# Kernel tuning notes

Measured on AMD Instinct MI355X. Metric: run time of the kernel, lower is better.

The kernel has to match this reference:

```python
import jax, jax.numpy as jnp
import numpy as np

N_NODES = 100000
N_EDGES = 1600000
D_IN = 128
D_OUT = 128


def setup_inputs() -> dict:
    key = jax.random.key(0)
    ks = jax.random.split(key, 6)
    x = jax.random.normal(ks[0], (N_NODES, D_IN), dtype=jnp.float32)
    edge_row = jax.random.randint(ks[1], (N_EDGES,), 0, N_NODES, dtype=jnp.int32)
    edge_col = jax.random.randint(ks[2], (N_EDGES,), 0, N_NODES, dtype=jnp.int32)
    # normalized adjacency values (e.g. 1/deg), roughly uniform small positives
    edge_val = jax.random.uniform(ks[3], (N_EDGES,), dtype=jnp.float32) * (1.0 / 16.0)
    # torch Linear weight is [out,in]; we store transposed [in,out] for x @ W
    scale = float(np.sqrt(6.0 / (D_IN + D_OUT)))  # xavier_uniform
    W_local = jax.random.uniform(ks[4], (D_IN, D_OUT), dtype=jnp.float32, minval=-scale, maxval=scale)
    W_neigh = jax.random.uniform(ks[5], (D_IN, D_OUT), dtype=jnp.float32, minval=-scale, maxval=scale)
    b_local = jnp.zeros((D_OUT,), dtype=jnp.float32)
    b_neigh = jnp.zeros((D_OUT,), dtype=jnp.float32)
    return {"x": x, "edge_row": edge_row, "edge_col": edge_col, "edge_val": edge_val,
            "W_local": W_local, "b_local": b_local, "W_neigh": W_neigh, "b_neigh": b_neigh}


def reference(x, edge_row, edge_col, edge_val, W_local, b_local, W_neigh, b_neigh):
    # feat_trans_local = linear_local(x)
    local = x @ W_local + b_local  # [N, D_OUT]
    # sparse.mm(edge_norm, x): out[r] += val * x[c]  (COO SpMM via gather + segment_sum)
    msgs = edge_val[:, None] * x[edge_col]  # [E, D_IN]
    agg = jax.ops.segment_sum(msgs, edge_row, num_segments=N_NODES)  # [N, D_IN]
    neigh = agg @ W_neigh + b_neigh  # [N, D_OUT]
    out = jnp.concatenate([local, neigh], axis=1)  # [N, 2*D_OUT]
    return jax.nn.relu(out)
```

## Files before the change

kernel.cpp:

```cpp
#include <hip/hip_runtime.h>
#include <hip/hip_bf16.h>

#define D 128
#define WPAD 136
#define RPC 64
#define RPC_SHIFT 6
#define CAPC 1280
#define NCMAX 2048
#define P1_BLOCKS 256

typedef __attribute__((ext_vector_type(8))) short short8;
typedef __attribute__((ext_vector_type(4))) short sh4;
typedef __attribute__((ext_vector_type(8))) __bf16 bf16x8;
typedef __attribute__((ext_vector_type(4))) float float4_t;

__device__ __forceinline__ short f2bf(float f) {
    __hip_bfloat16 b = __float2bfloat16(f);
    return __builtin_bit_cast(short, b);
}

__device__ __forceinline__ short8 load_frag8(const float* p) {
    const float4_t* q = reinterpret_cast<const float4_t*>(p);
    float4_t u = q[0], v = q[1];
    short8 r;
    r[0] = f2bf(u[0]); r[1] = f2bf(u[1]); r[2] = f2bf(u[2]); r[3] = f2bf(u[3]);
    r[4] = f2bf(v[0]); r[5] = f2bf(v[1]); r[6] = f2bf(v[2]); r[7] = f2bf(v[3]);
    return r;
}

__device__ __forceinline__ float4_t mfma_bf16(short8 a, short8 b, float4_t c) {
    return __builtin_amdgcn_mfma_f32_16x16x32_bf16(
        __builtin_bit_cast(bf16x8, a), __builtin_bit_cast(bf16x8, b), c, 0, 0, 0);
}

__device__ __forceinline__ float bf_lo(unsigned u) { return __uint_as_float(u << 16); }
__device__ __forceinline__ float bf_hi(unsigned u) { return __uint_as_float(u & 0xFFFF0000u); }

__global__ __launch_bounds__(256) void fused_gemm_scatter(
    const float* __restrict__ x,
    const float* __restrict__ Wl, const float* __restrict__ bl,
    const float* __restrict__ Wn,
    const int* __restrict__ erow, const int* __restrict__ ecol,
    const float* __restrict__ eval,
    float* __restrict__ out, unsigned short* __restrict__ y,
    int* __restrict__ gcur, int2* __restrict__ pairs1,
    int E, int ncoarse, int N)
{
    __shared__ int smem[D * WPAD / 2];

    if (blockIdx.x < P1_BLOCKS) {
        int* hist = smem;
        int* base = smem + NCMAX;
        int tid = threadIdx.x;
        for (int i = tid; i < ncoarse; i += 256) hist[i] = 0;
        __syncthreads();

        int chunk = (E + P1_BLOCKS - 1) / P1_BLOCKS;
        int e0 = blockIdx.x * chunk;
        int e1 = e0 + chunk; e1 = e1 < E ? e1 : E;

        for (int e = e0 + tid; e < e1; e += 256)
            atomicAdd(&hist[erow[e] >> RPC_SHIFT], 1);
        __syncthreads();

        for (int i = tid; i < ncoarse; i += 256) {
            int h = hist[i];
            base[i] = h ? atomicAdd(&gcur[i], h) : 0;
            hist[i] = 0;
        }
        __syncthreads();

        for (int e = e0 + tid; e < e1; e += 256) {
            int r = erow[e];
            int c = r >> RPC_SHIFT;
            int pos = atomicAdd(&hist[c], 1) + base[c];
            if (pos < CAPC) {
                int key = ((r & (RPC - 1)) << 17) | ecol[e];
                pairs1[(size_t)c * CAPC + pos] = make_int2(key, __float_as_int(eval[e]));
            }
        }
        return;
    }

    short* lW = reinterpret_cast<short*>(smem);
    int gb = blockIdx.x - P1_BLOCKS;

    for (int i = threadIdx.x; i < D * D; i += 256) {
        int k = i >> 7, n = i & (D - 1);
        lW[n * WPAD + k] = f2bf(Wl[i]);
    }

    int wave = threadIdx.x >> 6;
    int lane = threadIdx.x & 63;
    int quad = lane >> 4;
    int l16  = lane & 15;
    int rbase = gb * 128 + wave * 32;

    short8 ax[2][4];
    for (int m = 0; m < 2; ++m) {
        int row  = rbase + m * 16 + l16;
        int rowc = row < N ? row : N - 1;
        const float* xp = x + (size_t)rowc * D + quad * 8;
        for (int t = 0; t < 4; ++t) ax[m][t] = load_frag8(xp + t * 32);
    }
    __syncthreads();

    for (int nt = 0; nt < 8; ++nt) {
        int colc = nt * 16 + l16;
        float4_t acc0 = {0.f, 0.f, 0.f, 0.f};
        float4_t acc1 = {0.f, 0.f, 0.f, 0.f};
        const short* bp = lW + colc * WPAD + quad * 8;
        for (int t = 0; t < 4; ++t) {
            short8 bf = *reinterpret_cast<const short8*>(bp + t * 32);
            acc0 = mfma_bf16(bf, ax[0][t], acc0);
            acc1 = mfma_bf16(bf, ax[1][t], acc1);
        }
        float4_t blv = *reinterpret_cast<const float4_t*>(bl + nt * 16 + quad * 4);
        int col0 = nt * 16 + quad * 4;
        for (int m = 0; m < 2; ++m) {
            int row = rbase + m * 16 + l16;
            if (row < N) {
                float4_t a = m ? acc1 : acc0;
                float4_t ov;
                #pragma unroll
                for (int i = 0; i < 4; ++i) {
                    float lv = a[i] + blv[i];
                    ov[i] = lv > 0.f ? lv : 0.f;
                }
                *reinterpret_cast<float4_t*>(out + (size_t)row * 256 + col0) = ov;
            }
        }
    }
    __syncthreads();

    for (int i = threadIdx.x; i < D * D; i += 256) {
        int k = i >> 7, n = i & (D - 1);
        lW[n * WPAD + k] = f2bf(Wn[i]);
    }
    __syncthreads();

    for (int nt = 0; nt < 8; ++nt) {
        int colc = nt * 16 + l16;
        float4_t acc0 = {0.f, 0.f, 0.f, 0.f};
        float4_t acc1 = {0.f, 0.f, 0.f, 0.f};
        const short* bp = lW + colc * WPAD + quad * 8;
        for (int t = 0; t < 4; ++t) {
            short8 bf = *reinterpret_cast<const short8*>(bp + t * 32);
            acc0 = mfma_bf16(bf, ax[0][t], acc0);
            acc1 = mfma_bf16(bf, ax[1][t], acc1);
        }
        int col0 = nt * 16 + quad * 4;
        for (int m = 0; m < 2; ++m) {
            int row = rbase + m * 16 + l16;
            if (row < N) {
                float4_t a = m ? acc1 : acc0;
                sh4 s;
                #pragma unroll
                for (int i = 0; i < 4; ++i) s[i] = f2bf(a[i]);
                *reinterpret_cast<sh4*>(y + (size_t)row * 128 + col0) = s;
            }
        }
    }
}

__global__ __launch_bounds__(256) void bucket_gather(
    const unsigned short* __restrict__ y, const int* __restrict__ gcur,
    const int2* __restrict__ pairs1, const float* __restrict__ bn,
    float* __restrict__ out, int N)
{
    __shared__ unsigned short bidx[CAPC];
    __shared__ int hist[32];
    __shared__ int off[32];
    __shared__ int cur[32];

    int tid  = threadIdx.x;
    int wave = tid >> 6;
    int lane = tid & 63;
    int b    = blockIdx.x;
    int c    = b >> 1;
    int half = b & 1;

    if (tid < 32) { hist[tid] = 0; cur[tid] = 0; }
    __syncthreads();

    int cnt = gcur[c];
    cnt = cnt < CAPC ? cnt : CAPC;
    const int2* pb = pairs1 + (size_t)c * CAPC;

    for (int j = tid; j < cnt; j += 256) {
        int g = (pb[j].x >> 17) & (RPC - 1);
        if ((g >> 5) == half) atomicAdd(&hist[g & 31], 1);
    }
    __syncthreads();

    if (tid == 0) {
        int run = 0;
        for (int g = 0; g < 32; ++g) { off[g] = run; run += hist[g]; }
    }
    __syncthreads();

    for (int j = tid; j < cnt; j += 256) {
        int g = (pb[j].x >> 17) & (RPC - 1);
        if ((g >> 5) == half) {
            int pos = atomicAdd(&cur[g & 31], 1) + off[g & 31];
            bidx[pos] = (unsigned short)j;
        }
    }
    __syncthreads();

    const unsigned* yv = reinterpret_cast<const unsigned*>(y);
    float2 bnv = reinterpret_cast<const float2*>(bn)[lane];

    for (int rr = 0; rr < 8; ++rr) {
        int gl = wave * 8 + rr;
        int j0 = off[gl];
        int n  = hist[gl];
        float a0x = 0.f, a0y = 0.f, a1x = 0.f, a1y = 0.f;
        int j = 0;
        for (; j + 7 < n; j += 8) {
            int2 p[8];
            unsigned t[8];
            #pragma unroll
            for (int u = 0; u < 8; ++u) p[u] = pb[bidx[j0 + j + u]];
            #pragma unroll
            for (int u = 0; u < 8; ++u)
                t[u] = yv[(size_t)(p[u].x & 0x1FFFF) * 64 + lane];
            #pragma unroll
            for (int u = 0; u < 8; ++u) {
                float v = __int_as_float(p[u].y);
                if (u & 1) { a1x += v * bf_lo(t[u]); a1y += v * bf_hi(t[u]); }
                else       { a0x += v * bf_lo(t[u]); a0y += v * bf_hi(t[u]); }
            }
        }
        for (; j < n; ++j) {
            int2 p = pb[bidx[j0 + j]];
            unsigned t = yv[(size_t)(p.x & 0x1FFFF) * 64 + lane];
            float v = __int_as_float(p.y);
            a0x += v * bf_lo(t); a0y += v * bf_hi(t);
        }
        int node = c * RPC + half * 32 + gl;
        if (node < N) {
            float s0 = a0x + a1x + bnv.x;
            float s1 = a0y + a1y + bnv.y;
            float2 ov;
            ov.x = s0 > 0.f ? s0 : 0.f;
            ov.y = s1 > 0.f ? s1 : 0.f;
            reinterpret_cast<float2*>(out + (size_t)node * 256 + D)[lane] = ov;
        }
    }
}

extern "C" void kernel_launch(void* const* d_in, const int* in_sizes, int n_in,
                              void* d_out, int out_size, void* d_ws, size_t ws_size,
                              hipStream_t stream) {
    const float* x    = (const float*)d_in[0];
    const int*   erow = (const int*)  d_in[1];
    const int*   ecol = (const int*)  d_in[2];
    const float* eval = (const float*)d_in[3];
    const float* Wl   = (const float*)d_in[4];
    const float* bl   = (const float*)d_in[5];
    const float* Wn   = (const float*)d_in[6];
    const float* bn   = (const float*)d_in[7];
    float*       out  = (float*)d_out;

    int N = in_sizes[0] / D;
    int E = in_sizes[1];
    int ncoarse = (N + RPC - 1) >> RPC_SHIFT;

    char* ws = (char*)d_ws;
    size_t off_y   = 0;
    size_t off_p1  = off_y  + (size_t)N * D * sizeof(short);
    size_t off_gc  = off_p1 + (size_t)ncoarse * CAPC * sizeof(int2);

    unsigned short* y = (unsigned short*)(ws + off_y);
    int2* pairs1 = (int2*)(ws + off_p1);
    int*  gcur   = (int*)(ws + off_gc);

    hipMemsetAsync(gcur, 0, (size_t)ncoarse * sizeof(int), stream);

    int gblocks = (N + 127) / 128;
    fused_gemm_scatter<<<P1_BLOCKS + gblocks, 256, 0, stream>>>(
        x, Wl, bl, Wn, erow, ecol, eval, out, y, gcur, pairs1, E, ncoarse, N);

    bucket_gather<<<ncoarse * 2, 256, 0, stream>>>(y, gcur, pairs1, bn, out, N);
}
```

Measured before the change: 324.5 us.

## Use one block per coarse bucket and stream edges across row boundaries per wave

The gather kernel now launches one block per 64-row bucket instead of two half-buckets, so each bucket's pair list is scanned and histogrammed once rather than twice. Each wave processes its 16 rows as one contiguous run of sorted edges with a 16-wide load batch, flushing the accumulator whenever the row changes. This removes the per-row loop boundaries and padding tails. Rows with no edges get a default relu(bias) write afterwards. The cost is half as many blocks and a serial dependency through a single accumulator pair, with branchy flush logic inside the unrolled body.

Measured after the change: 317.2 us. -2.2%, faster.

```diff
diff --git a/kernel.cpp b/kernel.cpp
--- a/kernel.cpp
+++ b/kernel.cpp
@@ -169,83 +169,123 @@
     float* __restrict__ out, int N)
 {
     __shared__ unsigned short bidx[CAPC];
-    __shared__ int hist[32];
-    __shared__ int off[32];
-    __shared__ int cur[32];
+    __shared__ int hist[RPC];
+    __shared__ int off[RPC];
+    __shared__ int cur[RPC];
 
     int tid  = threadIdx.x;
     int wave = tid >> 6;
     int lane = tid & 63;
-    int b    = blockIdx.x;
-    int c    = b >> 1;
-    int half = b & 1;
-
-    if (tid < 32) { hist[tid] = 0; cur[tid] = 0; }
+    int c    = blockIdx.x;
+
+    if (tid < RPC) { hist[tid] = 0; cur[tid] = 0; }
     __syncthreads();
 
     int cnt = gcur[c];
     cnt = cnt < CAPC ? cnt : CAPC;
     const int2* pb = pairs1 + (size_t)c * CAPC;
 
+    for (int j = tid; j < cnt; j += 256)
+        atomicAdd(&hist[(pb[j].x >> 17) & (RPC - 1)], 1);
+    __syncthreads();
+
+    if (tid == 0) {
+        int run = 0;
+        for (int g = 0; g < RPC; ++g) { off[g] = run; run += hist[g]; }
+    }
+    __syncthreads();
+
     for (int j = tid; j < cnt; j += 256) {
         int g = (pb[j].x >> 17) & (RPC - 1);
-        if ((g >> 5) == half) atomicAdd(&hist[g & 31], 1);
-    }
-    __syncthreads();
-
-    if (tid == 0) {
-        int run = 0;
-        for (int g = 0; g < 32; ++g) { off[g] = run; run += hist[g]; }
-    }
-    __syncthreads();
-
-    for (int j = tid; j < cnt; j += 256) {
-        int g = (pb[j].x >> 17) & (RPC - 1);
-        if ((g >> 5) == half) {
-            int pos = atomicAdd(&cur[g & 31], 1) + off[g & 31];
-            bidx[pos] = (unsigned short)j;
-        }
+        int pos = atomicAdd(&cur[g], 1) + off[g];
+        bidx[pos] = (unsigned short)j;
     }
     __syncthreads();
 
     const unsigned* yv = reinterpret_cast<const unsigned*>(y);
     float2 bnv = reinterpret_cast<const float2*>(bn)[lane];
-
-    for (int rr = 0; rr < 8; ++rr) {
-        int gl = wave * 8 + rr;
-        int j0 = off[gl];
-        int n  = hist[gl];
-        float a0x = 0.f, a0y = 0.f, a1x = 0.f, a1y = 0.f;
-        int j = 0;
-        for (; j + 7 < n; j += 8) {
-            int2 p[8];
-            unsigned t[8];
-            #pragma unroll
-            for (int u = 0; u < 8; ++u) p[u] = pb[bidx[j0 + j + u]];
-            #pragma unroll
-            for (int u = 0; u < 8; ++u)
-                t[u] = yv[(size_t)(p[u].x & 0x1FFFF) * 64 + lane];
-            #pragma unroll
-            for (int u = 0; u < 8; ++u) {
-                float v = __int_as_float(p[u].y);
-                if (u & 1) { a1x += v * bf_lo(t[u]); a1y += v * bf_hi(t[u]); }
-                else       { a0x += v * bf_lo(t[u]); a0y += v * bf_hi(t[u]); }
+    float dflx = bnv.x > 0.f ? bnv.x : 0.f;
+    float dfly = bnv.y > 0.f ? bnv.y : 0.f;
+
+    int g0   = wave * 16;
+    int jbeg = off[g0];
+    int jend = (g0 + 16 < RPC) ? off[g0 + 16] : cnt;
+
+    unsigned seen = 0;
+    int   curg = -1;
+    float ax = 0.f, ay = 0.f;
+    int nodeb = c * RPC;
+
+#define CONSUME(P, T)                                                        \
+    {                                                                        \
+        int g = ((unsigned)(P).x >> 17) & (RPC - 1);                         \
+        if (g != curg) {                                                     \
+            if (curg >= 0) {                                                 \
+                float s0 = ax + bnv.x, s1 = ay + bnv.y;                      \
+                float2 ov;                                                   \
+                ov.x = s0 > 0.f ? s0 : 0.f;                                  \
+                ov.y = s1 > 0.f ? s1 : 0.f;                                  \
+                reinterpret_cast<float2*>(out + (size_t)(nodeb + curg) * 256 + D)[lane] = ov; \
+            }                                                                \
+            curg = g; seen |= 1u << (g - g0); ax = 0.f; ay = 0.f;            \
+        }                                                                    \
+        float v = __int_as_float((P).y);                                     \
+        ax += v * bf_lo(T); ay += v * bf_hi(T);                              \
+    }
+
+    int j = jbeg;
+    for (; j + 15 < jend; j += 16) {
+        int2 pA0, pA1, pA2, pA3, pA4, pA5, pA6, pA7;
+        int2 pB0, pB1, pB2, pB3, pB4, pB5, pB6, pB7;
+        pA0 = pb[bidx[j]];      pA1 = pb[bidx[j + 1]];
+        pA2 = pb[bidx[j + 2]];  pA3 = pb[bidx[j + 3]];
+        pA4 = pb[bidx[j + 4]];  pA5 = pb[bidx[j + 5]];
+        pA6 = pb[bidx[j + 6]];  pA7 = pb[bidx[j + 7]];
+        pB0 = pb[bidx[j + 8]];  pB1 = pb[bidx[j + 9]];
+        pB2 = pb[bidx[j + 10]]; pB3 = pb[bidx[j + 11]];
+        pB4 = pb[bidx[j + 12]]; pB5 = pb[bidx[j + 13]];
+        pB6 = pb[bidx[j + 14]]; pB7 = pb[bidx[j + 15]];
+        unsigned tA0 = yv[(size_t)(pA0.x & 0x1FFFF) * 64 + lane];
+        unsigned tA1 = yv[(size_t)(pA1.x & 0x1FFFF) * 64 + lane];
+        unsigned tA2 = yv[(size_t)(pA2.x & 0x1FFFF) * 64 + lane];
+        unsigned tA3 = yv[(size_t)(pA3.x & 0x1FFFF) * 64 + lane];
+        unsigned tA4 = yv[(size_t)(pA4.x & 0x1FFFF) * 64 + lane];
+        unsigned tA5 = yv[(size_t)(pA5.x & 0x1FFFF) * 64 + lane];
+        unsigned tA6 = yv[(size_t)(pA6.x & 0x1FFFF) * 64 + lane];
+        unsigned tA7 = yv[(size_t)(pA7.x & 0x1FFFF) * 64 + lane];
+        unsigned tB0 = yv[(size_t)(pB0.x & 0x1FFFF) * 64 + lane];
+        unsigned tB1 = yv[(size_t)(pB1.x & 0x1FFFF) * 64 + lane];
+        unsigned tB2 = yv[(size_t)(pB2.x & 0x1FFFF) * 64 + lane];
+        unsigned tB3 = yv[(size_t)(pB3.x & 0x1FFFF) * 64 + lane];
+        unsigned tB4 = yv[(size_t)(pB4.x & 0x1FFFF) * 64 + lane];
+        unsigned tB5 = yv[(size_t)(pB5.x & 0x1FFFF) * 64 + lane];
+        unsigned tB6 = yv[(size_t)(pB6.x & 0x1FFFF) * 64 + lane];
+        unsigned tB7 = yv[(size_t)(pB7.x & 0x1FFFF) * 64 + lane];
+        CONSUME(pA0, tA0) CONSUME(pA1, tA1) CONSUME(pA2, tA2) CONSUME(pA3, tA3)
+        CONSUME(pA4, tA4) CONSUME(pA5, tA5) CONSUME(pA6, tA6) CONSUME(pA7, tA7)
+        CONSUME(pB0, tB0) CONSUME(pB1, tB1) CONSUME(pB2, tB2) CONSUME(pB3, tB3)
+        CONSUME(pB4, tB4) CONSUME(pB5, tB5) CONSUME(pB6, tB6) CONSUME(pB7, tB7)
+    }
+    for (; j < jend; ++j) {
+        int2 p = pb[bidx[j]];
+        unsigned t = yv[(size_t)(p.x & 0x1FFFF) * 64 + lane];
+        CONSUME(p, t)
+    }
+#undef CONSUME
+    if (curg >= 0) {
+        float s0 = ax + bnv.x, s1 = ay + bnv.y;
+        float2 ov;
+        ov.x = s0 > 0.f ? s0 : 0.f;
+        ov.y = s1 > 0.f ? s1 : 0.f;
+        reinterpret_cast<float2*>(out + (size_t)(nodeb + curg) * 256 + D)[lane] = ov;
+    }
+    for (int g = 0; g < 16; ++g) {
+        if (!((seen >> g) & 1)) {
+            int node = nodeb + g0 + g;
+            if (node < N) {
+                float2 ov; ov.x = dflx; ov.y = dfly;
+                reinterpret_cast<float2*>(out + (size_t)node * 256 + D)[lane] = ov;
             }
-        }
-        for (; j < n; ++j) {
-            int2 p = pb[bidx[j0 + j]];
-            unsigned t = yv[(size_t)(p.x & 0x1FFFF) * 64 + lane];
-            float v = __int_as_float(p.y);
-            a0x += v * bf_lo(t); a0y += v * bf_hi(t);
-        }
-        int node = c * RPC + half * 32 + gl;
-        if (node < N) {
-            float s0 = a0x + a1x + bnv.x;
-            float s1 = a0y + a1y + bnv.y;
-            float2 ov;
-            ov.x = s0 > 0.f ? s0 : 0.f;
-            ov.y = s1 > 0.f ? s1 : 0.f;
-            reinterpret_cast<float2*>(out + (size_t)node * 256 + D)[lane] = ov;
         }
     }
 }
@@ -282,5 +322,5 @@
     fused_gemm_scatter<<<P1_BLOCKS + gblocks, 256, 0, stream>>>(
         x, Wl, bl, Wn, erow, ecol, eval, out, y, gcur, pairs1, E, ncoarse, N);
 
-    bucket_gather<<<ncoarse * 2, 256, 0, stream>>>(y, gcur, pairs1, bn, out, N);
-}
+    bucket_gather<<<ncoarse, 256, 0, stream>>>(y, gcur, pairs1, bn, out, N);
+}
```
